# Kernel optimization log

Hardware: AMD Instinct MI355X
Metric: run time of the kernel (lower is better)

Reference implementation:

```python
import jax, jax.numpy as jnp
import numpy as np

NEG_SLOPE = 0.2


def _build_dense_adj(edge_list, n):
    # edge_list: [2, E] int; symmetric 0/1 dense adjacency like edge_list_to_dense
    a = jnp.zeros((n, n), jnp.float32)
    a = a.at[edge_list[0], edge_list[1]].set(1.0)
    a = a.at[edge_list[1], edge_list[0]].set(1.0)
    return a


def setup_inputs() -> dict:
    key = jax.random.key(0)
    k1, k2, k3, k4 = jax.random.split(key, 4)
    N, T, D, H, E = 4096, 3, 16, 4, 65536
    scores = jax.random.normal(k1, (N, 1), jnp.float32)
    edge_type_emb = jax.random.normal(k2, (T, D), jnp.float32)
    att_w = jax.random.normal(k3, (H, D + 2, 1), jnp.float32) * 0.1  # xavier-ish
    edge_list = jax.random.randint(k4, (T, 2, E), 0, N, jnp.int64)
    return {"scores": scores, "edge_type_emb": edge_type_emb,
            "att_w": att_w, "edge_list": edge_list}


def reference(scores, edge_type_emb, att_w, edge_list):
    # scores: [N,1]; edge_type_emb: [T,D]; att_w: [H,D+2,1]; edge_list: [T,2,E]
    N = scores.shape[0]
    adjs = jax.vmap(lambda el: _build_dense_adj(el, N))(edge_list)  # [T,N,N]
    sum_adj = adjs.sum(axis=0)  # [N,N]
    s = scores[:, 0]            # [N]

    def head(w):
        w = w[:, 0]
        w_src, w_mid, w_tgt = w[0], w[1:-1], w[-1]
        # per-edge-type scalar from edge embedding dotted with middle weights
        c = edge_type_emb @ w_mid                    # [T]
        edge_term = jnp.einsum('tij,t->ij', adjs, c)  # [N,N]
        # (i,j): adj*(w_src*s_i) + adj*edge_emb.w_mid + adj*(w_tgt*s_j)
        logits = sum_adj * (w_src * s[:, None] + w_tgt * s[None, :]) + edge_term
        logits = jnp.where(logits >= 0, logits, NEG_SLOPE * logits)  # LeakyReLU
        att = jax.nn.softmax(logits, axis=-1)  # dense row softmax (as original)
        return att @ scores  # [N,1]

    outs = jax.vmap(head)(att_w)  # [H,N,1]
    return outs.mean(axis=0)      # average over heads
```

## Files before the change

### kernel.cpp

```cpp
#include <hip/hip_runtime.h>

#define NEG_SLOPE_F 0.2f

static constexpr int Nn = 4096;
static constexpr int Tt = 3;
static constexpr int Dd = 16;
static constexpr int Hh = 4;
static constexpr int CAP = 256;
static constexpr int WPR = 128;

__device__ __forceinline__ float waveMax(float v) {
#pragma unroll
  for (int m = 1; m < 64; m <<= 1) v = fmaxf(v, __shfl_xor(v, m));
  return v;
}
__device__ __forceinline__ float waveSum(float v) {
#pragma unroll
  for (int m = 1; m < 64; m <<= 1) v += __shfl_xor(v, m);
  return v;
}

__global__ void clear_prep_kernel(uint4* __restrict__ bm4,
                                  const float* __restrict__ scores,
                                  const float* __restrict__ emb,
                                  const float* __restrict__ attw,
                                  float* __restrict__ pv) {
  const int total = Nn * 3 * WPR / 4;
  uint4 z = make_uint4(0u, 0u, 0u, 0u);
  for (int k = blockIdx.x * 256 + threadIdx.x; k < total; k += gridDim.x * 256)
    bm4[k] = z;
  if (blockIdx.x == 0) {
    __shared__ float rb[4];
    int tid = threadIdx.x;
    float s = 0.f;
    for (int j = tid; j < Nn; j += 256) s += scores[j];
    s = waveSum(s);
    if ((tid & 63) == 0) rb[tid >> 6] = s;
    __syncthreads();
    if (tid == 0) pv[12] = rb[0] + rb[1] + rb[2] + rb[3];
    if (tid < Hh * Tt) {
      int h = tid / Tt, t = tid % Tt;
      float c = 0.f;
#pragma unroll
      for (int d = 0; d < Dd; ++d)
        c += emb[t * Dd + d] * attw[h * (Dd + 2) + 1 + d];
      pv[tid] = c;
    }
  }
}

__global__ void or_kernel(const int* __restrict__ el,
                          unsigned int* __restrict__ bitmap, int E) {
  int e = blockIdx.x * blockDim.x + threadIdx.x;
  if (e >= E) return;
  int t = blockIdx.y;
  unsigned int a = (unsigned int)el[(t * 2 + 0) * E + e];
  unsigned int b = (unsigned int)el[(t * 2 + 1) * E + e];
  atomicOr(&bitmap[(a * 3u + t) * WPR + (b >> 5)], 1u << (b & 31u));
  atomicOr(&bitmap[(b * 3u + t) * WPR + (a >> 5)], 1u << (a & 31u));
}

__launch_bounds__(256)
__global__ void row_kernel(const unsigned int* __restrict__ bitmap,
                           const float* __restrict__ scores,
                           const float* __restrict__ attw,
                           const float* __restrict__ pv,
                           float* __restrict__ out) {
  __shared__ unsigned short lst[4][CAP];
  int wid = threadIdx.x >> 6, lane = threadIdx.x & 63;
  int i = blockIdx.x * 4 + wid;
  const unsigned int* bm = bitmap + (size_t)i * 3 * WPR;

  unsigned int w[2][3];
#pragma unroll
  for (int p = 0; p < 2; ++p)
#pragma unroll
    for (int t = 0; t < 3; ++t) w[p][t] = bm[t * WPR + p * 64 + lane];
  unsigned int orw[2];
  orw[0] = w[0][0] | w[0][1] | w[0][2];
  orw[1] = w[1][0] | w[1][1] | w[1][2];
  int c = __popc(orw[0]) + __popc(orw[1]);
  int off = c;
#pragma unroll
  for (int d = 1; d < 64; d <<= 1) {
    int tv = __shfl_up(off, d);
    if (lane >= d) off += tv;
  }
  int n = __shfl(off, 63);
  off -= c;
  if (n > CAP) n = CAP;
  int idx = off;
#pragma unroll
  for (int p = 0; p < 2; ++p) {
    unsigned int o = orw[p];
    int jbase = (p * 64 + lane) * 32;
    while (o) {
      int b = __ffs(o) - 1;
      o &= o - 1;
      unsigned int m = ((w[p][0] >> b) & 1u) | (((w[p][1] >> b) & 1u) << 1) |
                       (((w[p][2] >> b) & 1u) << 2);
      if (idx < CAP) lst[wid][idx] = (unsigned short)((jbase + b) | (m << 12));
      ++idx;
    }
  }
  __syncthreads();

  float si = scores[i];
  float wsrc[Hh], wtgt[Hh], c0[Hh], c1[Hh], c2[Hh];
#pragma unroll
  for (int h = 0; h < Hh; ++h) {
    wsrc[h] = attw[h * (Dd + 2) + 0];
    wtgt[h] = attw[h * (Dd + 2) + Dd + 1];
    c0[h] = pv[h * 3 + 0];
    c1[h] = pv[h * 3 + 1];
    c2[h] = pv[h * 3 + 2];
  }
  float Ssum = pv[12];

  constexpr int IT = CAP / 64;
  float lv[IT][Hh], sjv[IT];
  float mx[Hh];
#pragma unroll
  for (int h = 0; h < Hh; ++h) mx[h] = -INFINITY;
  float sedge = 0.f;

#pragma unroll
  for (int it = 0; it < IT; ++it) {
    if (it * 64 >= n) break;
    int k = it * 64 + lane;
    bool act = k < n;
    unsigned int v = act ? (unsigned int)lst[wid][k] : 0u;
    int j = (int)(v & 0xFFFu);
    int m = act ? (int)(v >> 12) : 0;
    float sj = act ? scores[j] : 0.f;
    sjv[it] = sj;
    if (act) sedge += sj;
    float na = (float)__popc(m);
    float et0 = (m & 1) ? 1.f : 0.f;
    float et1 = (m & 2) ? 1.f : 0.f;
    float et2 = (m & 4) ? 1.f : 0.f;
#pragma unroll
    for (int h = 0; h < Hh; ++h) {
      float et = et0 * c0[h] + et1 * c1[h] + et2 * c2[h];
      float l = na * (wsrc[h] * si + wtgt[h] * sj) + et;
      l = (l >= 0.f) ? l : NEG_SLOPE_F * l;
      lv[it][h] = act ? l : -INFINITY;
      mx[h] = fmaxf(mx[h], lv[it][h]);
    }
  }

#pragma unroll
  for (int h = 0; h < Hh; ++h) {
    mx[h] = waveMax(mx[h]);
    if (n < Nn) mx[h] = fmaxf(mx[h], 0.f);
  }

  float se[Hh], ss[Hh];
#pragma unroll
  for (int h = 0; h < Hh; ++h) { se[h] = 0.f; ss[h] = 0.f; }
#pragma unroll
  for (int it = 0; it < IT; ++it) {
    if (it * 64 >= n) break;
#pragma unroll
    for (int h = 0; h < Hh; ++h) {
      float ex = expf(lv[it][h] - mx[h]);
      se[h] += ex;
      ss[h] += ex * sjv[it];
    }
  }
  sedge = waveSum(sedge);
#pragma unroll
  for (int h = 0; h < Hh; ++h) {
    se[h] = waveSum(se[h]);
    ss[h] = waveSum(ss[h]);
  }
  if (lane == 0) {
    float acc = 0.f;
#pragma unroll
    for (int h = 0; h < Hh; ++h) {
      float nz = expf(-mx[h]);
      float denom = se[h] + nz * ((float)Nn - (float)n);
      float numer = ss[h] + nz * (Ssum - sedge);
      acc += numer / denom;
    }
    out[i] = acc * (1.f / (float)Hh);
  }
}

extern "C" void kernel_launch(void* const* d_in, const int* in_sizes, int n_in,
                              void* d_out, int out_size, void* d_ws, size_t ws_size,
                              hipStream_t stream) {
  const float* scores = (const float*)d_in[0];
  const float* emb    = (const float*)d_in[1];
  const float* attw   = (const float*)d_in[2];
  const int*   el     = (const int*)d_in[3];
  float* out = (float*)d_out;
  int E = in_sizes[3] / (Tt * 2);

  size_t bm_bytes = (size_t)Nn * 3 * WPR * 4;
  unsigned int* bitmap = (unsigned int*)d_ws;
  float* pv = (float*)((char*)d_ws + bm_bytes);

  clear_prep_kernel<<<768, 256, 0, stream>>>((uint4*)d_ws, scores, emb, attw, pv);
  or_kernel<<<dim3((E + 255) / 256, Tt), 256, 0, stream>>>(el, bitmap, E);
  row_kernel<<<Nn / 4, 256, 0, stream>>>(bitmap, scores, attw, pv, out);
}
```

Baseline: 35.66 us.

## Replace global dense bitmap with per-row neighbor slot lists and LDS bitmap

Instead of clearing and atomically OR-ing a 6 MB global bitmap, edges are scattered into per-(row,type) slot lists of capacity 96 via atomicAdd counters. Each row wave then rebuilds its bitmap in shared memory from the slots before the existing compaction and softmax. This removes the large memset and the scattered global bitmap traffic, at the cost of a fixed slot capacity that silently drops neighbors if a row/type degree exceeds 96. The slot path may also store duplicate edges, which the LDS bitmap then dedups.

```diff
diff --git a/kernel.cpp b/kernel.cpp
--- a/kernel.cpp
+++ b/kernel.cpp
@@ -7,7 +7,7 @@
 static constexpr int Dd = 16;
 static constexpr int Hh = 4;
 static constexpr int CAP = 256;
-static constexpr int WPR = 128;
+static constexpr int BCAP = 96;
 
 __device__ __forceinline__ float waveMax(float v) {
 #pragma unroll
@@ -20,18 +20,16 @@
   return v;
 }
 
-__global__ void clear_prep_kernel(uint4* __restrict__ bm4,
+__global__ void clear_prep_kernel(unsigned int* __restrict__ cnt,
                                   const float* __restrict__ scores,
                                   const float* __restrict__ emb,
                                   const float* __restrict__ attw,
                                   float* __restrict__ pv) {
-  const int total = Nn * 3 * WPR / 4;
-  uint4 z = make_uint4(0u, 0u, 0u, 0u);
-  for (int k = blockIdx.x * 256 + threadIdx.x; k < total; k += gridDim.x * 256)
-    bm4[k] = z;
+  int tid = threadIdx.x;
+  int g = blockIdx.x * 256 + tid;
+  if (g < Nn * Tt) cnt[g] = 0u;
   if (blockIdx.x == 0) {
     __shared__ float rb[4];
-    int tid = threadIdx.x;
     float s = 0.f;
     for (int j = tid; j < Nn; j += 256) s += scores[j];
     s = waveSum(s);
@@ -49,33 +47,56 @@
   }
 }
 
-__global__ void or_kernel(const int* __restrict__ el,
-                          unsigned int* __restrict__ bitmap, int E) {
-  int e = blockIdx.x * blockDim.x + threadIdx.x;
-  if (e >= E) return;
-  int t = blockIdx.y;
+__global__ void scatter_kernel(const int* __restrict__ el,
+                               unsigned int* __restrict__ cnt,
+                               unsigned short* __restrict__ slots, int E) {
+  int k = blockIdx.x * blockDim.x + threadIdx.x;
+  if (k >= Tt * E) return;
+  int t = k / E, e = k - t * E;
   unsigned int a = (unsigned int)el[(t * 2 + 0) * E + e];
   unsigned int b = (unsigned int)el[(t * 2 + 1) * E + e];
-  atomicOr(&bitmap[(a * 3u + t) * WPR + (b >> 5)], 1u << (b & 31u));
-  atomicOr(&bitmap[(b * 3u + t) * WPR + (a >> 5)], 1u << (a & 31u));
+  unsigned int pa = atomicAdd(&cnt[a * Tt + t], 1u);
+  if (pa < BCAP) slots[(a * Tt + t) * BCAP + pa] = (unsigned short)b;
+  unsigned int pb = atomicAdd(&cnt[b * Tt + t], 1u);
+  if (pb < BCAP) slots[(b * Tt + t) * BCAP + pb] = (unsigned short)a;
 }
 
 __launch_bounds__(256)
-__global__ void row_kernel(const unsigned int* __restrict__ bitmap,
+__global__ void row_kernel(const unsigned int* __restrict__ cnt,
+                           const unsigned short* __restrict__ slots,
                            const float* __restrict__ scores,
                            const float* __restrict__ attw,
                            const float* __restrict__ pv,
                            float* __restrict__ out) {
+  __shared__ unsigned int bmL[4][Tt * 128];
   __shared__ unsigned short lst[4][CAP];
   int wid = threadIdx.x >> 6, lane = threadIdx.x & 63;
   int i = blockIdx.x * 4 + wid;
-  const unsigned int* bm = bitmap + (size_t)i * 3 * WPR;
+  unsigned int* bm = bmL[wid];
+
+  for (int q = lane; q < Tt * 128; q += 64) bm[q] = 0u;
+
+  int cv[Tt];
+#pragma unroll
+  for (int t = 0; t < Tt; ++t) {
+    int c = (int)cnt[i * Tt + t];
+    cv[t] = c < BCAP ? c : BCAP;
+  }
+  const unsigned short* sl = slots + (size_t)i * Tt * BCAP;
+  for (int k = lane; k < Tt * BCAP; k += 64) {
+    int t = k / BCAP, s = k - t * BCAP;
+    if (s < cv[t]) {
+      unsigned int j = (unsigned int)sl[k];
+      atomicOr(&bm[t * 128 + (j >> 5)], 1u << (j & 31u));
+    }
+  }
+  __syncthreads();
 
   unsigned int w[2][3];
 #pragma unroll
   for (int p = 0; p < 2; ++p)
 #pragma unroll
-    for (int t = 0; t < 3; ++t) w[p][t] = bm[t * WPR + p * 64 + lane];
+    for (int t = 0; t < 3; ++t) w[p][t] = bm[t * 128 + p * 64 + lane];
   unsigned int orw[2];
   orw[0] = w[0][0] | w[0][1] | w[0][2];
   orw[1] = w[1][0] | w[1][1] | w[1][2];
@@ -197,11 +218,12 @@
   float* out = (float*)d_out;
   int E = in_sizes[3] / (Tt * 2);
 
-  size_t bm_bytes = (size_t)Nn * 3 * WPR * 4;
-  unsigned int* bitmap = (unsigned int*)d_ws;
-  float* pv = (float*)((char*)d_ws + bm_bytes);
-
-  clear_prep_kernel<<<768, 256, 0, stream>>>((uint4*)d_ws, scores, emb, attw, pv);
-  or_kernel<<<dim3((E + 255) / 256, Tt), 256, 0, stream>>>(el, bitmap, E);
-  row_kernel<<<Nn / 4, 256, 0, stream>>>(bitmap, scores, attw, pv, out);
-}
+  unsigned int* cnt = (unsigned int*)d_ws;
+  float* pv = (float*)((char*)d_ws + (size_t)Nn * Tt * 4);
+  unsigned short* slots = (unsigned short*)((char*)pv + 64);
+
+  clear_prep_kernel<<<(Nn * Tt + 255) / 256, 256, 0, stream>>>(cnt, scores, emb,
+                                                               attw, pv);
+  scatter_kernel<<<(Tt * (E) + 255) / 256, 256, 0, stream>>>(el, cnt, slots, E);
+  row_kernel<<<Nn / 4, 256, 0, stream>>>(cnt, slots, scores, attw, pv, out);
+}
```

Measured after the change: 41.65 us. 16.8% more time.
